# Kernel tuning notes

Measured on AMD Instinct MI355X. Metric: run time of the kernel, lower is better.

Reference implementation:

```python
import jax, jax.numpy as jnp
import numpy as np

NS = 100000  # senders
NR = 100000  # receivers
E = 600000   # edges
D = 128      # sender_dim = receiver_dim = edge_dim
EPS = 1e-5


def _layer_norm(x, g, b):
    mu = jnp.mean(x, axis=-1, keepdims=True)
    var = jnp.mean(jnp.square(x - mu), axis=-1, keepdims=True)
    return (x - mu) * jax.lax.rsqrt(var + EPS) * g + b


def _gcast_mlp(x, W, b, gamma, beta):
    # Faithful to GCastMLP.forward: z = silu(linear(x)); z = LN(silu(z))
    z = jax.nn.silu(x @ W.T + b)
    return _layer_norm(jax.nn.silu(z), gamma, beta)


def setup_inputs() -> dict:
    key = jax.random.key(0)
    ks = jax.random.split(key, 12)
    s = 1.0 / np.sqrt(3 * D)
    inp = {
        "sender_x": jax.random.normal(ks[0], (NS, D), jnp.float32),
        "receiver_x": jax.random.normal(ks[1], (NR, D), jnp.float32),
        "edge_index": jax.random.randint(ks[2], (2, E), 0, NR, jnp.int32),
        "edge_attr": jax.random.normal(ks[3], (E, D), jnp.float32),
        # edge MLP: in = sender+receiver+edge = 3D, out = edge_dim
        "We": jax.random.uniform(ks[4], (D, 3 * D), jnp.float32, -s, s),
        "be": jnp.zeros((D,), jnp.float32),
        "ge": jnp.ones((D,), jnp.float32),
        "bbe": jnp.zeros((D,), jnp.float32),
        # node MLP: in = receiver+edge = 2D, out = receiver_dim
        "Wn": jax.random.uniform(ks[5], (D, 2 * D), jnp.float32, -1.0 / np.sqrt(2 * D), 1.0 / np.sqrt(2 * D)),
        "bn": jnp.zeros((D,), jnp.float32),
        "gn": jnp.ones((D,), jnp.float32),
        "bbn": jnp.zeros((D,), jnp.float32),
        # sender MLP: square D -> D
        "Ws": jax.random.uniform(ks[6], (D, D), jnp.float32, -1.0 / np.sqrt(D), 1.0 / np.sqrt(D)),
        "bs": jnp.zeros((D,), jnp.float32),
        "gs": jnp.ones((D,), jnp.float32),
        "bbs": jnp.zeros((D,), jnp.float32),
    }
    return inp


def reference(sender_x, receiver_x, edge_index, edge_attr,
              We, be, ge, bbe, Wn, bn, gn, bbn, Ws, bs, gs, bbs):
    src, dst = edge_index[0], edge_index[1]
    # Edge encoder: gather endpoints, concat, MLP -> new edge features [E, D]
    edge_in = jnp.concatenate([sender_x[src], receiver_x[dst], edge_attr], axis=-1)
    edge_attr_p = _gcast_mlp(edge_in, We, be, ge, bbe)
    # Node encoder: scatter-sum messages (= new edge features) to receivers
    edge_aggr = jax.ops.segment_sum(edge_attr_p, dst, num_segments=receiver_x.shape[0])
    mesh_x_p = _gcast_mlp(jnp.concatenate([receiver_x, edge_aggr], axis=-1), Wn, bn, gn, bbn)
    # Residual updates
    sender_out = sender_x + _gcast_mlp(sender_x, Ws, bs, gs, bbs)
    receiver_out = receiver_x + mesh_x_p
    edge_out = edge_attr + edge_attr_p
    return (sender_out, receiver_out, edge_out)
```

## Files before the change

kernel.cpp:

```cpp
#include <hip/hip_runtime.h>
#include <stdint.h>


typedef __bf16 bf16x8 __attribute__((ext_vector_type(8)));
typedef float  f32x4  __attribute__((ext_vector_type(4)));

union U16B { uint4 u; bf16x8 v; };
union BFPK { __bf16 h[2]; unsigned int u; };
union BF1  { __bf16 h; unsigned short s; };

__device__ __forceinline__ float silu_f(float x) {
  return x * __builtin_amdgcn_rcpf(1.0f + __expf(-x));
}
__device__ __forceinline__ float bfu2f(unsigned int lo16) {
  return __uint_as_float(lo16 << 16);
}
__device__ __forceinline__ bf16x8 cvt8(float4 a, float4 b) {
  bf16x8 r;
  r[0] = (__bf16)a.x; r[1] = (__bf16)a.y; r[2] = (__bf16)a.z; r[3] = (__bf16)a.w;
  r[4] = (__bf16)b.x; r[5] = (__bf16)b.y; r[6] = (__bf16)b.z; r[7] = (__bf16)b.w;
  return r;
}

__global__ void prep_kernel(const float* __restrict__ We,
                            const float* __restrict__ Wn,
                            const float* __restrict__ Ws,
                            unsigned short* __restrict__ wimg,
                            const float* __restrict__ sx,
                            unsigned short* __restrict__ sb,
                            const float* __restrict__ rx,
                            unsigned short* __restrict__ rb,
                            int n8s, int n8r,
                            const int* __restrict__ dst,
                            int* __restrict__ counts, int E) {
  int i = blockIdx.x * 256 + threadIdx.x;
  if (i < 6 * 16384) {
    int panel = i >> 14;
    int r = (i >> 7) & 127;
    int csw = i & 127;
    int c_or = ((csw * 2) ^ ((r & 15) << 4)) >> 1;
    float f;
    if (panel < 3)      f = We[r * 384 + panel * 128 + c_or];
    else if (panel < 5) f = Wn[r * 256 + (panel - 3) * 128 + c_or];
    else                f = Ws[r * 128 + c_or];
    BF1 c; c.h = (__bf16)f;
    wimg[i] = c.s;
    return;
  }
  int j = i - 6 * 16384;
  if (j < n8s + n8r) {
    const float* in; unsigned short* out; int idx;
    if (j < n8s) { in = sx; out = sb; idx = j; }
    else         { in = rx; out = rb; idx = j - n8s; }
    float4 a = reinterpret_cast<const float4*>(in)[2 * idx];
    float4 b = reinterpret_cast<const float4*>(in)[2 * idx + 1];
    U16B r8; r8.v = cvt8(a, b);
    reinterpret_cast<uint4*>(out)[idx] = r8.u;
    return;
  }
  int e = j - n8s - n8r;
  if (e < E) atomicAdd(&counts[dst[e]], 1);
}

__global__ void scan1_kernel(const int* __restrict__ counts, int* __restrict__ pre,
                             int* __restrict__ blockSums, int n) {
  __shared__ int sh[256];
  const int t = threadIdx.x;
  const int base = blockIdx.x * 1024 + t * 4;
  int c0 = (base + 0 < n) ? counts[base + 0] : 0;
  int c1 = (base + 1 < n) ? counts[base + 1] : 0;
  int c2 = (base + 2 < n) ? counts[base + 2] : 0;
  int c3 = (base + 3 < n) ? counts[base + 3] : 0;
  int tot = c0 + c1 + c2 + c3;
  sh[t] = tot;
  __syncthreads();
  #pragma unroll
  for (int off = 1; off < 256; off <<= 1) {
    int v = (t >= off) ? sh[t - off] : 0;
    __syncthreads();
    sh[t] += v;
    __syncthreads();
  }
  int excl = sh[t] - tot;
  if (base + 0 < n) pre[base + 0] = excl;
  if (base + 1 < n) pre[base + 1] = excl + c0;
  if (base + 2 < n) pre[base + 2] = excl + c0 + c1;
  if (base + 3 < n) pre[base + 3] = excl + c0 + c1 + c2;
  if (t == 255) blockSums[blockIdx.x] = sh[255];
}

__global__ void scan2_kernel(int* __restrict__ blockSums, int nb) {
  __shared__ int sh[512];
  const int t = threadIdx.x;
  int v = (t < nb) ? blockSums[t] : 0;
  sh[t] = v;
  __syncthreads();
  #pragma unroll
  for (int off = 1; off < 512; off <<= 1) {
    int u = (t >= off) ? sh[t - off] : 0;
    __syncthreads();
    sh[t] += u;
    __syncthreads();
  }
  if (t < nb) blockSums[t] = sh[t] - v;
}

__global__ void scan3_kernel(const int* __restrict__ pre, const int* __restrict__ blockSums,
                             int* __restrict__ offs, int* __restrict__ cursor, int n) {
  int i = blockIdx.x * 256 + threadIdx.x;
  if (i >= n) return;
  int o = pre[i] + blockSums[i >> 10];
  offs[i] = o;
  cursor[i] = o;
}

__global__ void scatter_kernel(const int* __restrict__ dst, int* __restrict__ cursor,
                               int* __restrict__ rank, int E) {
  int i = blockIdx.x * 256 + threadIdx.x;
  if (i < E) {
    int p = atomicAdd(&cursor[dst[i]], 1);
    rank[i] = p;
  }
}

__global__ __launch_bounds__(256) void agg_kernel(
    const unsigned short* __restrict__ P,
    const int* __restrict__ offs, const int* __restrict__ counts,
    unsigned short* __restrict__ aggr, int NR) {
  const int l = threadIdx.x & 31;
  const int g0 = (blockIdx.x * 256 + threadIdx.x) >> 5;
  if (g0 >= NR) return;
  int beg = offs[g0];
  int cnt = counts[g0];
  float s0 = 0.f, s1 = 0.f, s2 = 0.f, s3 = 0.f;
  const unsigned short* p = P + (size_t)beg * 128 + l * 4;
  for (int k = 0; k < cnt; ++k) {
    uint2 w = *reinterpret_cast<const uint2*>(p);
    p += 128;
    s0 += bfu2f(w.x & 0xffffu);
    s1 += bfu2f(w.x >> 16);
    s2 += bfu2f(w.y & 0xffffu);
    s3 += bfu2f(w.y >> 16);
  }
  BFPK a, b;
  a.h[0] = (__bf16)s0; a.h[1] = (__bf16)s1;
  b.h[0] = (__bf16)s2; b.h[1] = (__bf16)s3;
  uint2 o; o.x = a.u; o.y = b.u;
  *reinterpret_cast<uint2*>(aggr + (size_t)g0 * 128 + l * 4) = o;
}

template <int KDIM, int AGGR>
__global__ __launch_bounds__(512, 6) void mlp_v10_kernel(
    const unsigned short* __restrict__ s0, const int* __restrict__ i0,
    const unsigned short* __restrict__ s1, const int* __restrict__ i1,
    const float* __restrict__ s2,
    const unsigned short* __restrict__ Wb,
    const float* __restrict__ bias, const float* __restrict__ gamma,
    const float* __restrict__ beta,
    const float* __restrict__ resid,
    float* __restrict__ outp,
    void* aggr, const int* __restrict__ aggr_idx,
    const int* __restrict__ prank,
    int M) {
  constexpr int NSEG = KDIM / 128;
  __shared__ __align__(16) unsigned short smem[16384];

  const int tid = threadIdx.x;
  const int wid = tid >> 6;
  const int lane = tid & 63;
  const int l15 = lane & 15;
  const int q = lane >> 4;
  const int l31 = lane & 31;
  const int rhalf = lane >> 5;
  const int wrow = blockIdx.x * 128 + wid * 16;
  const int xm = l15 << 3;

  int rr = wrow + l15;
  if (rr >= M) rr = M - 1;
  const unsigned short* p0 = s0 + (size_t)(i0 ? i0[rr] : rr) * 128;
  const unsigned short* p1 = nullptr;
  const float* p2 = nullptr;
  if constexpr (KDIM >= 256) p1 = s1 + (size_t)(i1 ? i1[rr] : rr) * 128;
  if constexpr (KDIM >= 384) p2 = s2 + (size_t)rr * 128;

  auto stageB = [&](int seg) {
    const unsigned short* g = Wb + seg * 16384 + wid * 2048 + lane * 8;
    unsigned short* l = &smem[wid * 2048];
    #pragma unroll
    for (int u = 0; u < 4; ++u) {
      __builtin_amdgcn_global_load_lds(
          (const __attribute__((address_space(1))) unsigned int*)(g + u * 512),
          (__attribute__((address_space(3))) unsigned int*)(l + u * 512),
          16, 0, 0);
    }
  };

  U16B Ac[4], An[4];
  auto loadA = [&](int seg, U16B (&dst)[4]) {
    #pragma unroll
    for (int k4 = 0; k4 < 4; ++k4) {
      const int kof = k4 * 32 + q * 8;
      if (seg == 0) {
        dst[k4].u = *reinterpret_cast<const uint4*>(p0 + kof);
      } else if (seg == 1) {
        dst[k4].u = *reinterpret_cast<const uint4*>(p1 + kof);
      } else {
        const float4* p = reinterpret_cast<const float4*>(p2 + kof);
        dst[k4].v = cvt8(p[0], p[1]);
      }
    }
  };

  f32x4 acc[8] = {};

  stageB(0);
  loadA(0, Ac);
  __syncthreads();

  #pragma unroll
  for (int seg = 0; seg < NSEG; ++seg) {
    if (seg + 1 < NSEG) loadA(seg + 1, An);
    #pragma unroll
    for (int k4 = 0; k4 < 4; ++k4) {
      #pragma unroll
      for (int n = 0; n < 8; ++n) {
        U16B b;
        b.u = *reinterpret_cast<const uint4*>(
            &smem[(n * 16 + l15) * 128 + ((k4 * 32 + q * 8) ^ xm)]);
        acc[n] = __builtin_amdgcn_mfma_f32_16x16x32_bf16(Ac[k4].v, b.v, acc[n], 0, 0, 0);
      }
    }
    __syncthreads();
    if (seg + 1 < NSEG) {
      stageB(seg + 1);
      __syncthreads();
      #pragma unroll
      for (int k4 = 0; k4 < 4; ++k4) Ac[k4] = An[k4];
    }
  }

  float bia[8];
  #pragma unroll
  for (int n = 0; n < 8; ++n) bia[n] = bias[n * 16 + l15];

  float sum[4] = {0.f, 0.f, 0.f, 0.f};
  float ssq[4] = {0.f, 0.f, 0.f, 0.f};
  #pragma unroll
  for (int n = 0; n < 8; ++n) {
    #pragma unroll
    for (int j = 0; j < 4; ++j) {
      float t = silu_f(silu_f(acc[n][j] + bia[n]));
      acc[n][j] = t;
      sum[j] += t;
      ssq[j] += t * t;
    }
  }
  #pragma unroll
  for (int off = 1; off < 16; off <<= 1) {
    #pragma unroll
    for (int j = 0; j < 4; ++j) {
      sum[j] += __shfl_xor(sum[j], off);
      ssq[j] += __shfl_xor(ssq[j], off);
    }
  }
  float mu[4], rs[4];
  #pragma unroll
  for (int j = 0; j < 4; ++j) {
    mu[j] = sum[j] * (1.0f / 128.0f);
    float var = ssq[j] * (1.0f / 128.0f) - mu[j] * mu[j];
    rs[j] = rsqrtf(var + 1e-5f);
  }
  float gam[8], bet[8];
  #pragma unroll
  for (int n = 0; n < 8; ++n) {
    gam[n] = gamma[n * 16 + l15];
    bet[n] = beta[n * 16 + l15];
  }

  unsigned short* yw = &smem[wid * 2048];

  #pragma unroll
  for (int h = 0; h < 2; ++h) {
    if (h == 1) {
      asm volatile("s_waitcnt lgkmcnt(0)" ::: "memory");
    }
    if ((q >> 1) == h) {
      #pragma unroll
      for (int n = 0; n < 8; ++n) {
        #pragma unroll
        for (int j = 0; j < 4; ++j) {
          float y = (acc[n][j] - mu[j]) * rs[j] * gam[n] + bet[n];
          BF1 c; c.h = (__bf16)y;
          yw[((q & 1) * 4 + j) * 132 + n * 16 + l15] = c.s;
        }
      }
    }
    asm volatile("s_waitcnt lgkmcnt(0)" ::: "memory");

    #pragma unroll
    for (int s = 0; s < 4; ++s) {
      int row8 = 2 * s + rhalf;
      int grow = wrow + 8 * h + row8;
      uint2 w = *reinterpret_cast<const uint2*>(&yw[row8 * 132 + l31 * 4]);
      if (grow < M) {
        const f32x4 r4 = *reinterpret_cast<const f32x4*>(resid + (size_t)grow * 128 + l31 * 4);
        f32x4 o4;
        o4.x = r4.x + bfu2f(w.x & 0xffffu);
        o4.y = r4.y + bfu2f(w.x >> 16);
        o4.z = r4.z + bfu2f(w.y & 0xffffu);
        o4.w = r4.w + bfu2f(w.y >> 16);
        __builtin_nontemporal_store(o4, reinterpret_cast<f32x4*>(outp + (size_t)grow * 128 + l31 * 4));
        if constexpr (AGGR == 3) {
          int prow = prank[grow];
          *reinterpret_cast<uint2*>((unsigned short*)aggr + (size_t)prow * 128 + l31 * 4) = w;
        } else if constexpr (AGGR == 2) {
          int idx = aggr_idx[grow];
          unsigned short* ar = (unsigned short*)aggr + (size_t)idx * 128 + l31 * 4;
          asm volatile("global_atomic_pk_add_bf16 %0, %1, off" :: "v"(ar), "v"(w.x) : "memory");
          asm volatile("global_atomic_pk_add_bf16 %0, %1, off" :: "v"(ar + 2), "v"(w.y) : "memory");
        }
      }
    }
  }
}

template <int KDIM>
__global__ __launch_bounds__(512, 4) void mlp_fb_kernel(
    const float* __restrict__ s0, const int* __restrict__ i0,
    const float* __restrict__ s1, const int* __restrict__ i1,
    const float* __restrict__ s2,
    const unsigned short* __restrict__ Wb,
    const float* __restrict__ bias, const float* __restrict__ gamma,
    const float* __restrict__ beta,
    const float* __restrict__ resid,
    float* __restrict__ outp,
    float* aggr, const int* __restrict__ aggr_idx,
    int M) {
  constexpr int NSEG = KDIM / 128;
  __shared__ __align__(16) unsigned short smem[2][16384];
  const int tid = threadIdx.x;
  const int wid = tid >> 6;
  const int lane = tid & 63;
  const int l15 = lane & 15;
  const int q = lane >> 4;
  const int l31 = lane & 31;
  const int rhalf = lane >> 5;
  const int wrow = blockIdx.x * 128 + wid * 16;
  const int xm = l15 << 3;

  int rr = wrow + l15;
  if (rr >= M) rr = M - 1;
  const float* p0 = s0 + (size_t)(i0 ? i0[rr] : rr) * 128;
  const float* p1 = (KDIM >= 256) ? (s1 + (size_t)(i1 ? i1[rr] : rr) * 128) : nullptr;
  const float* p2 = (KDIM >= 384) ? (s2 + (size_t)rr * 128) : nullptr;

  auto stageB = [&](int seg, int buf) {
    const unsigned short* g = Wb + seg * 16384 + wid * 2048 + lane * 8;
    unsigned short* l = &smem[buf][wid * 2048];
    #pragma unroll
    for (int u = 0; u < 4; ++u) {
      __builtin_amdgcn_global_load_lds(
          (const __attribute__((address_space(1))) unsigned int*)(g + u * 512),
          (__attribute__((address_space(3))) unsigned int*)(l + u * 512),
          16, 0, 0);
    }
  };

  stageB(0, 0);
  f32x4 acc[8] = {};
  __syncthreads();
  int cur = 0;
  #pragma unroll
  for (int seg = 0; seg < NSEG; ++seg) {
    if (seg + 1 < NSEG) stageB(seg + 1, cur ^ 1);
    const float* base = (seg == 0) ? p0 : ((seg == 1) ? p1 : p2);
    #pragma unroll
    for (int k4 = 0; k4 < 4; ++k4) {
      const float4* pp = reinterpret_cast<const float4*>(base + k4 * 32 + q * 8);
      U16B a; a.v = cvt8(pp[0], pp[1]);
      #pragma unroll
      for (int n = 0; n < 8; ++n) {
        U16B b;
        b.u = *reinterpret_cast<const uint4*>(
            &smem[cur][(n * 16 + l15) * 128 + ((k4 * 32 + q * 8) ^ xm)]);
        acc[n] = __builtin_amdgcn_mfma_f32_16x16x32_bf16(a.v, b.v, acc[n], 0, 0, 0);
      }
    }
    __syncthreads();
    if (seg + 1 < NSEG) cur ^= 1;
  }

  unsigned short* yw = &smem[0][0] + wid * (16 * 132);
  float bia[8];
  #pragma unroll
  for (int n = 0; n < 8; ++n) bia[n] = bias[n * 16 + l15];
  float sum[4] = {0.f, 0.f, 0.f, 0.f}, ssq[4] = {0.f, 0.f, 0.f, 0.f};
  #pragma unroll
  for (int n = 0; n < 8; ++n)
    #pragma unroll
    for (int j = 0; j < 4; ++j) {
      float t = silu_f(silu_f(acc[n][j] + bia[n]));
      acc[n][j] = t; sum[j] += t; ssq[j] += t * t;
    }
  #pragma unroll
  for (int off = 1; off < 16; off <<= 1)
    #pragma unroll
    for (int j = 0; j < 4; ++j) {
      sum[j] += __shfl_xor(sum[j], off);
      ssq[j] += __shfl_xor(ssq[j], off);
    }
  float mu[4], rs[4];
  #pragma unroll
  for (int j = 0; j < 4; ++j) {
    mu[j] = sum[j] * (1.0f / 128.0f);
    float var = ssq[j] * (1.0f / 128.0f) - mu[j] * mu[j];
    rs[j] = rsqrtf(var + 1e-5f);
  }
  float gam[8], bet[8];
  #pragma unroll
  for (int n = 0; n < 8; ++n) { gam[n] = gamma[n * 16 + l15]; bet[n] = beta[n * 16 + l15]; }
  #pragma unroll
  for (int n = 0; n < 8; ++n)
    #pragma unroll
    for (int j = 0; j < 4; ++j) {
      float y = (acc[n][j] - mu[j]) * rs[j] * gam[n] + bet[n];
      BF1 c; c.h = (__bf16)y;
      yw[(q * 4 + j) * 132 + n * 16 + l15] = c.s;
    }
  asm volatile("s_waitcnt lgkmcnt(0)" ::: "memory");
  #pragma unroll
  for (int s = 0; s < 8; ++s) {
    int row16 = 2 * s + rhalf;
    int grow = wrow + row16;
    uint2 w = *reinterpret_cast<const uint2*>(&yw[row16 * 132 + l31 * 4]);
    if (grow < M) {
      const f32x4 r4 = *reinterpret_cast<const f32x4*>(resid + (size_t)grow * 128 + l31 * 4);
      f32x4 o4;
      o4.x = r4.x + bfu2f(w.x & 0xffffu);
      o4.y = r4.y + bfu2f(w.x >> 16);
      o4.z = r4.z + bfu2f(w.y & 0xffffu);
      o4.w = r4.w + bfu2f(w.y >> 16);
      __builtin_nontemporal_store(o4, reinterpret_cast<f32x4*>(outp + (size_t)grow * 128 + l31 * 4));
      if (aggr) {
        int idx = aggr_idx[grow];
        float* ar = aggr + (size_t)idx * 128 + l31 * 4;
        atomicAdd(ar + 0, bfu2f(w.x & 0xffffu));
        atomicAdd(ar + 1, bfu2f(w.x >> 16));
        atomicAdd(ar + 2, bfu2f(w.y & 0xffffu));
        atomicAdd(ar + 3, bfu2f(w.y >> 16));
      }
    }
  }
}

extern "C" void kernel_launch(void* const* d_in, const int* in_sizes, int n_in,
                              void* d_out, int out_size, void* d_ws, size_t ws_size,
                              hipStream_t stream) {
  const float* sender_x   = (const float*)d_in[0];
  const float* receiver_x = (const float*)d_in[1];
  const int*   edge_index = (const int*)d_in[2];
  const float* edge_attr  = (const float*)d_in[3];
  const float* We  = (const float*)d_in[4];
  const float* be  = (const float*)d_in[5];
  const float* ge  = (const float*)d_in[6];
  const float* bbe = (const float*)d_in[7];
  const float* Wn  = (const float*)d_in[8];
  const float* bn  = (const float*)d_in[9];
  const float* gn  = (const float*)d_in[10];
  const float* bbn = (const float*)d_in[11];
  const float* Ws  = (const float*)d_in[12];
  const float* bs  = (const float*)d_in[13];
  const float* gs  = (const float*)d_in[14];
  const float* bbs = (const float*)d_in[15];

  const int D  = 128;
  const int NS = in_sizes[0] / D;
  const int NR = in_sizes[1] / D;
  const int E  = in_sizes[2] / 2;

  const int* src = edge_index;
  const int* dst = edge_index + E;

  float* out          = (float*)d_out;
  float* sender_out   = out;
  float* receiver_out = out + (size_t)NS * D;
  float* edge_out     = out + (size_t)(NS + NR) * D;

  const size_t welems = 6 * 16384;
  unsigned short* We_b = (unsigned short*)d_ws;
  unsigned short* Wn_b = We_b + 3 * 16384;
  unsigned short* Ws_b = We_b + 5 * 16384;
  unsigned short* sender_b   = We_b + welems;
  unsigned short* receiver_b = sender_b + (size_t)NS * D;
  unsigned short* aggr_b     = receiver_b + (size_t)NR * D;
  unsigned short* P_b        = aggr_b + (size_t)NR * D;
  int* counts    = (int*)(P_b + (size_t)E * D);
  int* pre       = counts + NR;
  int* offs      = pre + NR;
  int* cursor    = offs + NR;
  int* blockSums = cursor + NR;
  int* rank      = blockSums + 512;

  const int nScanBlocks = (NR + 1023) / 1024;
  const size_t needCSR = 2 * (welems + (size_t)(NS + 2 * NR) * D + (size_t)E * D)
                       + 4 * (4 * (size_t)NR + 512 + (size_t)E);
  const size_t needA = (welems + (size_t)(NS + 2 * NR) * D) * 2;

  int tier;
  if (ws_size >= needCSR && nScanBlocks <= 512) tier = 0;
  else if (ws_size >= needA) tier = 1;
  else tier = 2;

  const int gridE = (E + 127) / 128;
  const int gridR = (NR + 127) / 128;
  const int gridS = (NS + 127) / 128;
  const int n8s = NS * D / 8, n8r = NR * D / 8;

  if (tier == 0) {
    (void)hipMemsetAsync(counts, 0, (size_t)NR * 4, stream);
    const int prepItems = (int)welems + n8s + n8r + E;
    prep_kernel<<<(prepItems + 255) / 256, 256, 0, stream>>>(
        We, Wn, Ws, We_b, sender_x, sender_b, receiver_x, receiver_b,
        n8s, n8r, dst, counts, E);

    scan1_kernel<<<nScanBlocks, 256, 0, stream>>>(counts, pre, blockSums, NR);
    scan2_kernel<<<1, 512, 0, stream>>>(blockSums, nScanBlocks);
    scan3_kernel<<<(NR + 255) / 256, 256, 0, stream>>>(pre, blockSums, offs, cursor, NR);
    scatter_kernel<<<(E + 255) / 256, 256, 0, stream>>>(dst, cursor, rank, E);

    mlp_v10_kernel<384, 3><<<gridE, 512, 0, stream>>>(
        sender_b, src, receiver_b, dst, edge_attr,
        We_b, be, ge, bbe, edge_attr, edge_out, P_b, nullptr, rank, E);

    agg_kernel<<<(NR + 7) / 8, 256, 0, stream>>>(P_b, offs, counts, aggr_b, NR);

    mlp_v10_kernel<256, 0><<<gridR, 512, 0, stream>>>(
        receiver_b, nullptr, aggr_b, nullptr, nullptr,
        Wn_b, bn, gn, bbn, receiver_x, receiver_out, nullptr, nullptr, nullptr, NR);

    mlp_v10_kernel<128, 0><<<gridS, 512, 0, stream>>>(
        sender_b, nullptr, nullptr, nullptr, nullptr,
        Ws_b, bs, gs, bbs, sender_x, sender_out, nullptr, nullptr, nullptr, NS);
  } else if (tier == 1) {
    const int prepItems = (int)welems + n8s + n8r;
    prep_kernel<<<(prepItems + 255) / 256, 256, 0, stream>>>(
        We, Wn, Ws, We_b, sender_x, sender_b, receiver_x, receiver_b,
        n8s, n8r, nullptr, nullptr, 0);
    (void)hipMemsetAsync(aggr_b, 0, (size_t)NR * D * 2, stream);

    mlp_v10_kernel<384, 2><<<gridE, 512, 0, stream>>>(
        sender_b, src, receiver_b, dst, edge_attr,
        We_b, be, ge, bbe, edge_attr, edge_out, aggr_b, dst, nullptr, E);

    mlp_v10_kernel<256, 0><<<gridR, 512, 0, stream>>>(
        receiver_b, nullptr, aggr_b, nullptr, nullptr,
        Wn_b, bn, gn, bbn, receiver_x, receiver_out, nullptr, nullptr, nullptr, NR);

    mlp_v10_kernel<128, 0><<<gridS, 512, 0, stream>>>(
        sender_b, nullptr, nullptr, nullptr, nullptr,
        Ws_b, bs, gs, bbs, sender_x, sender_out, nullptr, nullptr, nullptr, NS);
  } else {
    prep_kernel<<<(int)((welems + 255) / 256), 256, 0, stream>>>(
        We, Wn, Ws, We_b, nullptr, nullptr, nullptr, nullptr, 0, 0,
        nullptr, nullptr, 0);
    (void)hipMemsetAsync(receiver_out, 0, (size_t)NR * D * sizeof(float), stream);

    mlp_fb_kernel<384><<<gridE, 512, 0, stream>>>(
        sender_x, src, receiver_x, dst, edge_attr,
        We_b, be, ge, bbe, edge_attr, edge_out, receiver_out, dst, E);

    mlp_fb_kernel<256><<<gridR, 512, 0, stream>>>(
        receiver_x, nullptr, receiver_out, nullptr, nullptr,
        Wn_b, bn, gn, bbn, receiver_x, receiver_out, nullptr, nullptr, NR);

    mlp_fb_kernel<128><<<gridS, 512, 0, stream>>>(
        sender_x, nullptr, nullptr, nullptr, nullptr,
        Ws_b, bs, gs, bbs, sender_x, sender_out, nullptr, nullptr, NS);
  }
}
```

Measured before the change: 450.0 us.

## Precompute sender/receiver projections per node before edge MLP gather

Splits the edge linear layer by linearity: the sender and receiver blocks of We are applied once per node (100k rows each) in a new pregemm kernel, writing bf16 projections. The edge kernel then runs only a K=128 GEMM on edge_attr and adds gathered precomputed projections, instead of a K=384 GEMM on gathered raw features for 600k edges. This cuts edge MFMA work to a third. In exchange it adds an extra kernel, extra workspace, and a second bf16 rounding of the projected sender and receiver terms.

```diff
diff --git a/kernel.cpp b/kernel.cpp
--- a/kernel.cpp
+++ b/kernel.cpp
@@ -149,6 +149,189 @@
   *reinterpret_cast<uint2*>(aggr + (size_t)g0 * 128 + l * 4) = o;
 }
 
+__global__ __launch_bounds__(512, 4) void pregemm_kernel(
+    const unsigned short* __restrict__ Xs, const unsigned short* __restrict__ Xr,
+    const unsigned short* __restrict__ Wp0, const unsigned short* __restrict__ Wp1,
+    unsigned short* __restrict__ Sp, unsigned short* __restrict__ Rp,
+    int NSl, int NRl, int gridS) {
+  __shared__ __align__(16) unsigned short smem[16384];
+  const bool isR = ((int)blockIdx.x >= gridS);
+  const unsigned short* X  = isR ? Xr : Xs;
+  const unsigned short* Wp = isR ? Wp1 : Wp0;
+  unsigned short* OUT = isR ? Rp : Sp;
+  const int M = isR ? NRl : NSl;
+  const int b = isR ? ((int)blockIdx.x - gridS) : (int)blockIdx.x;
+
+  const int tid = threadIdx.x;
+  const int wid = tid >> 6;
+  const int lane = tid & 63;
+  const int l15 = lane & 15;
+  const int q = lane >> 4;
+  const int xm = l15 << 3;
+
+  int e = b * 128 + wid * 16 + l15;
+  const bool valid = (e < M);
+  if (!valid) e = M - 1;
+
+  {
+    const unsigned short* g = Wp + wid * 2048 + lane * 8;
+    unsigned short* l = &smem[wid * 2048];
+    #pragma unroll
+    for (int u = 0; u < 4; ++u) {
+      __builtin_amdgcn_global_load_lds(
+          (const __attribute__((address_space(1))) unsigned int*)(g + u * 512),
+          (__attribute__((address_space(3))) unsigned int*)(l + u * 512),
+          16, 0, 0);
+    }
+  }
+
+  U16B bfr[4];
+  const unsigned short* xp = X + (size_t)e * 128;
+  #pragma unroll
+  for (int k4 = 0; k4 < 4; ++k4)
+    bfr[k4].u = *reinterpret_cast<const uint4*>(xp + k4 * 32 + q * 8);
+
+  __syncthreads();
+
+  f32x4 acc[8] = {};
+  #pragma unroll
+  for (int k4 = 0; k4 < 4; ++k4) {
+    #pragma unroll
+    for (int n = 0; n < 8; ++n) {
+      U16B a;
+      a.u = *reinterpret_cast<const uint4*>(
+          &smem[(n * 16 + l15) * 128 + ((k4 * 32 + q * 8) ^ xm)]);
+      acc[n] = __builtin_amdgcn_mfma_f32_16x16x32_bf16(a.v, bfr[k4].v, acc[n], 0, 0, 0);
+    }
+  }
+
+  if (valid) {
+    #pragma unroll
+    for (int n = 0; n < 8; ++n) {
+      BFPK k0, k1;
+      k0.h[0] = (__bf16)acc[n][0]; k0.h[1] = (__bf16)acc[n][1];
+      k1.h[0] = (__bf16)acc[n][2]; k1.h[1] = (__bf16)acc[n][3];
+      uint2 w; w.x = k0.u; w.y = k1.u;
+      *reinterpret_cast<uint2*>(OUT + (size_t)e * 128 + n * 16 + q * 4) = w;
+    }
+  }
+}
+
+__global__ __launch_bounds__(512, 4) void edge_v11_kernel(
+    const float* __restrict__ edge_attr,
+    const int* __restrict__ src, const int* __restrict__ dst,
+    const unsigned short* __restrict__ Sp, const unsigned short* __restrict__ Rp,
+    const unsigned short* __restrict__ Wp,
+    const float* __restrict__ bias, const float* __restrict__ gamma,
+    const float* __restrict__ beta,
+    float* __restrict__ edge_out,
+    unsigned short* __restrict__ P, const int* __restrict__ prank,
+    int E) {
+  __shared__ __align__(16) unsigned short smem[16384];
+  const int tid = threadIdx.x;
+  const int wid = tid >> 6;
+  const int lane = tid & 63;
+  const int l15 = lane & 15;
+  const int q = lane >> 4;
+  const int xm = l15 << 3;
+
+  int e = blockIdx.x * 128 + wid * 16 + l15;
+  const bool valid = (e < E);
+  if (!valid) e = E - 1;
+
+  {
+    const unsigned short* g = Wp + wid * 2048 + lane * 8;
+    unsigned short* l = &smem[wid * 2048];
+    #pragma unroll
+    for (int u = 0; u < 4; ++u) {
+      __builtin_amdgcn_global_load_lds(
+          (const __attribute__((address_space(1))) unsigned int*)(g + u * 512),
+          (__attribute__((address_space(3))) unsigned int*)(l + u * 512),
+          16, 0, 0);
+    }
+  }
+
+  const float* ep = edge_attr + (size_t)e * 128;
+  U16B bfr[4];
+  #pragma unroll
+  for (int k4 = 0; k4 < 4; ++k4) {
+    const float4* p = reinterpret_cast<const float4*>(ep + k4 * 32 + q * 8);
+    bfr[k4].v = cvt8(p[0], p[1]);
+  }
+
+  const int se = src[e];
+  const int de = dst[e];
+  const int rk = prank[e];
+  uint2 Sg[8], Rg[8];
+  const unsigned short* sp = Sp + (size_t)se * 128 + q * 4;
+  const unsigned short* rp = Rp + (size_t)de * 128 + q * 4;
+  #pragma unroll
+  for (int n = 0; n < 8; ++n) {
+    Sg[n] = *reinterpret_cast<const uint2*>(sp + n * 16);
+    Rg[n] = *reinterpret_cast<const uint2*>(rp + n * 16);
+  }
+
+  __syncthreads();
+
+  f32x4 acc[8] = {};
+  #pragma unroll
+  for (int k4 = 0; k4 < 4; ++k4) {
+    #pragma unroll
+    for (int n = 0; n < 8; ++n) {
+      U16B a;
+      a.u = *reinterpret_cast<const uint4*>(
+          &smem[(n * 16 + l15) * 128 + ((k4 * 32 + q * 8) ^ xm)]);
+      acc[n] = __builtin_amdgcn_mfma_f32_16x16x32_bf16(a.v, bfr[k4].v, acc[n], 0, 0, 0);
+    }
+  }
+
+  float sum = 0.f, ssq = 0.f;
+  #pragma unroll
+  for (int n = 0; n < 8; ++n) {
+    const f32x4 b4 = *reinterpret_cast<const f32x4*>(bias + n * 16 + q * 4);
+    float sg0 = bfu2f(Sg[n].x & 0xffffu), sg1 = bfu2f(Sg[n].x >> 16);
+    float sg2 = bfu2f(Sg[n].y & 0xffffu), sg3 = bfu2f(Sg[n].y >> 16);
+    float rg0 = bfu2f(Rg[n].x & 0xffffu), rg1 = bfu2f(Rg[n].x >> 16);
+    float rg2 = bfu2f(Rg[n].y & 0xffffu), rg3 = bfu2f(Rg[n].y >> 16);
+    float z0 = acc[n][0] + b4[0] + sg0 + rg0;
+    float z1 = acc[n][1] + b4[1] + sg1 + rg1;
+    float z2 = acc[n][2] + b4[2] + sg2 + rg2;
+    float z3 = acc[n][3] + b4[3] + sg3 + rg3;
+    float t0 = silu_f(silu_f(z0));
+    float t1 = silu_f(silu_f(z1));
+    float t2 = silu_f(silu_f(z2));
+    float t3 = silu_f(silu_f(z3));
+    acc[n][0] = t0; acc[n][1] = t1; acc[n][2] = t2; acc[n][3] = t3;
+    sum += (t0 + t1) + (t2 + t3);
+    ssq += (t0 * t0 + t1 * t1) + (t2 * t2 + t3 * t3);
+  }
+  sum += __shfl_xor(sum, 16); ssq += __shfl_xor(ssq, 16);
+  sum += __shfl_xor(sum, 32); ssq += __shfl_xor(ssq, 32);
+  const float mu = sum * (1.0f / 128.0f);
+  const float rs = rsqrtf(ssq * (1.0f / 128.0f) - mu * mu + 1e-5f);
+
+  #pragma unroll
+  for (int n = 0; n < 8; ++n) {
+    const f32x4 g4  = *reinterpret_cast<const f32x4*>(gamma + n * 16 + q * 4);
+    const f32x4 be4 = *reinterpret_cast<const f32x4*>(beta + n * 16 + q * 4);
+    const f32x4 r4  = *reinterpret_cast<const f32x4*>(ep + n * 16 + q * 4);
+    f32x4 y;
+    #pragma unroll
+    for (int j = 0; j < 4; ++j)
+      y[j] = (acc[n][j] - mu) * rs * g4[j] + be4[j];
+    if (valid) {
+      f32x4 o4 = r4 + y;
+      __builtin_nontemporal_store(
+          o4, reinterpret_cast<f32x4*>(edge_out + (size_t)e * 128 + n * 16 + q * 4));
+      BFPK k0, k1;
+      k0.h[0] = (__bf16)y[0]; k0.h[1] = (__bf16)y[1];
+      k1.h[0] = (__bf16)y[2]; k1.h[1] = (__bf16)y[3];
+      uint2 w; w.x = k0.u; w.y = k1.u;
+      *reinterpret_cast<uint2*>(P + (size_t)rk * 128 + n * 16 + q * 4) = w;
+    }
+  }
+}
+
 template <int KDIM, int AGGR>
 __global__ __launch_bounds__(512, 6) void mlp_v10_kernel(
     const unsigned short* __restrict__ s0, const int* __restrict__ i0,
@@ -500,23 +683,27 @@
   int* cursor    = offs + NR;
   int* blockSums = cursor + NR;
   int* rank      = blockSums + 512;
+  unsigned short* Sp = (unsigned short*)(rank + E);
+  unsigned short* Rp = Sp + (size_t)NS * D;
 
   const int nScanBlocks = (NR + 1023) / 1024;
   const size_t needCSR = 2 * (welems + (size_t)(NS + 2 * NR) * D + (size_t)E * D)
                        + 4 * (4 * (size_t)NR + 512 + (size_t)E);
+  const size_t needCSR2 = needCSR + 2 * ((size_t)(NS + NR) * D);
   const size_t needA = (welems + (size_t)(NS + 2 * NR) * D) * 2;
 
   int tier;
-  if (ws_size >= needCSR && nScanBlocks <= 512) tier = 0;
-  else if (ws_size >= needA) tier = 1;
-  else tier = 2;
+  if (ws_size >= needCSR2 && nScanBlocks <= 512) tier = 0;
+  else if (ws_size >= needCSR && nScanBlocks <= 512) tier = 1;
+  else if (ws_size >= needA) tier = 2;
+  else tier = 3;
 
   const int gridE = (E + 127) / 128;
   const int gridR = (NR + 127) / 128;
   const int gridS = (NS + 127) / 128;
   const int n8s = NS * D / 8, n8r = NR * D / 8;
 
-  if (tier == 0) {
+  if (tier <= 1) {
     (void)hipMemsetAsync(counts, 0, (size_t)NR * 4, stream);
     const int prepItems = (int)welems + n8s + n8r + E;
     prep_kernel<<<(prepItems + 255) / 256, 256, 0, stream>>>(
@@ -528,9 +715,18 @@
     scan3_kernel<<<(NR + 255) / 256, 256, 0, stream>>>(pre, blockSums, offs, cursor, NR);
     scatter_kernel<<<(E + 255) / 256, 256, 0, stream>>>(dst, cursor, rank, E);
 
-    mlp_v10_kernel<384, 3><<<gridE, 512, 0, stream>>>(
-        sender_b, src, receiver_b, dst, edge_attr,
-        We_b, be, ge, bbe, edge_attr, edge_out, P_b, nullptr, rank, E);
+    if (tier == 0) {
+      pregemm_kernel<<<gridS + gridR, 512, 0, stream>>>(
+          sender_b, receiver_b, We_b, We_b + 16384, Sp, Rp, NS, NR, gridS);
+
+      edge_v11_kernel<<<gridE, 512, 0, stream>>>(
+          edge_attr, src, dst, Sp, Rp, We_b + 2 * 16384,
+          be, ge, bbe, edge_out, P_b, rank, E);
+    } else {
+      mlp_v10_kernel<384, 3><<<gridE, 512, 0, stream>>>(
+          sender_b, src, receiver_b, dst, edge_attr,
+          We_b, be, ge, bbe, edge_attr, edge_out, P_b, nullptr, rank, E);
+    }
 
     agg_kernel<<<(NR + 7) / 8, 256, 0, stream>>>(P_b, offs, counts, aggr_b, NR);
 
@@ -541,7 +737,7 @@
     mlp_v10_kernel<128, 0><<<gridS, 512, 0, stream>>>(
         sender_b, nullptr, nullptr, nullptr, nullptr,
         Ws_b, bs, gs, bbs, sender_x, sender_out, nullptr, nullptr, nullptr, NS);
-  } else if (tier == 1) {
+  } else if (tier == 2) {
     const int prepItems = (int)welems + n8s + n8r;
     prep_kernel<<<(prepItems + 255) / 256, 256, 0, stream>>>(
         We, Wn, Ws, We_b, sender_x, sender_b, receiver_x, receiver_b,
```

New measurement: 537.3 us. 19.4% more time.

## Fuse CSR aggregation into node MLP and merge edge and sender MLP launches

Applied to the files above, without the earlier changes.

Removes the separate agg_kernel and instead gathers each receiver's CSR-sorted edge messages directly into the A-operand registers of a new node MLP kernel, which skips writing and re-reading the bf16 aggregate buffer. The receiver-half GEMM is issued first so the second weight segment can load while the aggregation loop runs. The edge MLP and sender MLP are also merged into one launch that picks its path by block index, cutting launches and filling the tail of the edge grid. In exchange, the node kernel does one per-row gather loop per lane group with uneven degree across rows, uses more registers (launch bounds 512,4), and may have lower memory-level parallelism than the old dedicated aggregation kernel.

```diff
diff --git a/kernel.cpp b/kernel.cpp
--- a/kernel.cpp
+++ b/kernel.cpp
@@ -123,34 +123,9 @@
   }
 }
 
-__global__ __launch_bounds__(256) void agg_kernel(
-    const unsigned short* __restrict__ P,
-    const int* __restrict__ offs, const int* __restrict__ counts,
-    unsigned short* __restrict__ aggr, int NR) {
-  const int l = threadIdx.x & 31;
-  const int g0 = (blockIdx.x * 256 + threadIdx.x) >> 5;
-  if (g0 >= NR) return;
-  int beg = offs[g0];
-  int cnt = counts[g0];
-  float s0 = 0.f, s1 = 0.f, s2 = 0.f, s3 = 0.f;
-  const unsigned short* p = P + (size_t)beg * 128 + l * 4;
-  for (int k = 0; k < cnt; ++k) {
-    uint2 w = *reinterpret_cast<const uint2*>(p);
-    p += 128;
-    s0 += bfu2f(w.x & 0xffffu);
-    s1 += bfu2f(w.x >> 16);
-    s2 += bfu2f(w.y & 0xffffu);
-    s3 += bfu2f(w.y >> 16);
-  }
-  BFPK a, b;
-  a.h[0] = (__bf16)s0; a.h[1] = (__bf16)s1;
-  b.h[0] = (__bf16)s2; b.h[1] = (__bf16)s3;
-  uint2 o; o.x = a.u; o.y = b.u;
-  *reinterpret_cast<uint2*>(aggr + (size_t)g0 * 128 + l * 4) = o;
-}
-
 template <int KDIM, int AGGR>
-__global__ __launch_bounds__(512, 6) void mlp_v10_kernel(
+__device__ __forceinline__ void mlp_core(
+    unsigned short* smem,
     const unsigned short* __restrict__ s0, const int* __restrict__ i0,
     const unsigned short* __restrict__ s1, const int* __restrict__ i1,
     const float* __restrict__ s2,
@@ -161,9 +136,8 @@
     float* __restrict__ outp,
     void* aggr, const int* __restrict__ aggr_idx,
     const int* __restrict__ prank,
-    int M) {
+    int M, int bid) {
   constexpr int NSEG = KDIM / 128;
-  __shared__ __align__(16) unsigned short smem[16384];
 
   const int tid = threadIdx.x;
   const int wid = tid >> 6;
@@ -172,7 +146,7 @@
   const int q = lane >> 4;
   const int l31 = lane & 31;
   const int rhalf = lane >> 5;
-  const int wrow = blockIdx.x * 128 + wid * 16;
+  const int wrow = bid * 128 + wid * 16;
   const int xm = l15 << 3;
 
   int rr = wrow + l15;
@@ -319,6 +293,229 @@
           asm volatile("global_atomic_pk_add_bf16 %0, %1, off" :: "v"(ar), "v"(w.x) : "memory");
           asm volatile("global_atomic_pk_add_bf16 %0, %1, off" :: "v"(ar + 2), "v"(w.y) : "memory");
         }
+      }
+    }
+  }
+}
+
+template <int KDIM, int AGGR>
+__global__ __launch_bounds__(512, 6) void mlp_v10_kernel(
+    const unsigned short* __restrict__ s0, const int* __restrict__ i0,
+    const unsigned short* __restrict__ s1, const int* __restrict__ i1,
+    const float* __restrict__ s2,
+    const unsigned short* __restrict__ Wb,
+    const float* __restrict__ bias, const float* __restrict__ gamma,
+    const float* __restrict__ beta,
+    const float* __restrict__ resid,
+    float* __restrict__ outp,
+    void* aggr, const int* __restrict__ aggr_idx,
+    const int* __restrict__ prank,
+    int M) {
+  __shared__ __align__(16) unsigned short smem[16384];
+  mlp_core<KDIM, AGGR>(smem, s0, i0, s1, i1, s2, Wb, bias, gamma, beta,
+                       resid, outp, aggr, aggr_idx, prank, M, blockIdx.x);
+}
+
+__global__ __launch_bounds__(512, 6) void fused_es_kernel(
+    const unsigned short* __restrict__ sender_b, const int* __restrict__ src,
+    const unsigned short* __restrict__ receiver_b, const int* __restrict__ dst,
+    const float* __restrict__ edge_attr,
+    const unsigned short* __restrict__ We_b,
+    const float* __restrict__ be, const float* __restrict__ ge,
+    const float* __restrict__ bbe,
+    float* __restrict__ edge_out,
+    unsigned short* __restrict__ P, const int* __restrict__ rank,
+    const unsigned short* __restrict__ Ws_b,
+    const float* __restrict__ bs, const float* __restrict__ gs,
+    const float* __restrict__ bbs,
+    const float* __restrict__ sender_x, float* __restrict__ sender_out,
+    int E, int NS, int gridE) {
+  __shared__ __align__(16) unsigned short smem[16384];
+  const int b = blockIdx.x;
+  if (b < gridE) {
+    mlp_core<384, 3>(smem, sender_b, src, receiver_b, dst, edge_attr,
+                     We_b, be, ge, bbe, edge_attr, edge_out,
+                     P, nullptr, rank, E, b);
+  } else {
+    mlp_core<128, 0>(smem, sender_b, nullptr, nullptr, nullptr, nullptr,
+                     Ws_b, bs, gs, bbs, sender_x, sender_out,
+                     nullptr, nullptr, nullptr, NS, b - gridE);
+  }
+}
+
+__global__ __launch_bounds__(512, 4) void node_csr_kernel(
+    const unsigned short* __restrict__ s0,
+    const unsigned short* __restrict__ P,
+    const int* __restrict__ offs, const int* __restrict__ counts,
+    const unsigned short* __restrict__ Wb,
+    const float* __restrict__ bias, const float* __restrict__ gamma,
+    const float* __restrict__ beta,
+    const float* __restrict__ resid, float* __restrict__ outp,
+    int M) {
+  __shared__ __align__(16) unsigned short smem[16384];
+
+  const int tid = threadIdx.x;
+  const int wid = tid >> 6;
+  const int lane = tid & 63;
+  const int l15 = lane & 15;
+  const int q = lane >> 4;
+  const int l31 = lane & 31;
+  const int rhalf = lane >> 5;
+  const int wrow = blockIdx.x * 128 + wid * 16;
+  const int xm = l15 << 3;
+
+  int rr = wrow + l15;
+  if (rr >= M) rr = M - 1;
+  const unsigned short* p0 = s0 + (size_t)rr * 128;
+
+  auto stageB = [&](int seg) {
+    const unsigned short* g = Wb + seg * 16384 + wid * 2048 + lane * 8;
+    unsigned short* l = &smem[wid * 2048];
+    #pragma unroll
+    for (int u = 0; u < 4; ++u) {
+      __builtin_amdgcn_global_load_lds(
+          (const __attribute__((address_space(1))) unsigned int*)(g + u * 512),
+          (__attribute__((address_space(3))) unsigned int*)(l + u * 512),
+          16, 0, 0);
+    }
+  };
+
+  U16B Ac[4];
+  #pragma unroll
+  for (int k4 = 0; k4 < 4; ++k4)
+    Ac[k4].u = *reinterpret_cast<const uint4*>(p0 + k4 * 32 + q * 8);
+
+  stageB(0);
+  __syncthreads();
+
+  f32x4 acc[8] = {};
+  #pragma unroll
+  for (int k4 = 0; k4 < 4; ++k4) {
+    #pragma unroll
+    for (int n = 0; n < 8; ++n) {
+      U16B b;
+      b.u = *reinterpret_cast<const uint4*>(
+          &smem[(n * 16 + l15) * 128 + ((k4 * 32 + q * 8) ^ xm)]);
+      acc[n] = __builtin_amdgcn_mfma_f32_16x16x32_bf16(Ac[k4].v, b.v, acc[n], 0, 0, 0);
+    }
+  }
+  __syncthreads();
+  stageB(1);
+
+  {
+    int beg = offs[rr];
+    int cnt = counts[rr];
+    float a32[32];
+    #pragma unroll
+    for (int t = 0; t < 32; ++t) a32[t] = 0.f;
+    const unsigned short* prow = P + (size_t)beg * 128;
+    for (int k = 0; k < cnt; ++k) {
+      #pragma unroll
+      for (int k4 = 0; k4 < 4; ++k4) {
+        uint4 w = *reinterpret_cast<const uint4*>(prow + k4 * 32 + q * 8);
+        a32[k4 * 8 + 0] += bfu2f(w.x & 0xffffu);
+        a32[k4 * 8 + 1] += bfu2f(w.x >> 16);
+        a32[k4 * 8 + 2] += bfu2f(w.y & 0xffffu);
+        a32[k4 * 8 + 3] += bfu2f(w.y >> 16);
+        a32[k4 * 8 + 4] += bfu2f(w.z & 0xffffu);
+        a32[k4 * 8 + 5] += bfu2f(w.z >> 16);
+        a32[k4 * 8 + 6] += bfu2f(w.w & 0xffffu);
+        a32[k4 * 8 + 7] += bfu2f(w.w >> 16);
+      }
+      prow += 128;
+    }
+    #pragma unroll
+    for (int k4 = 0; k4 < 4; ++k4) {
+      #pragma unroll
+      for (int j = 0; j < 8; ++j)
+        Ac[k4].v[j] = (__bf16)a32[k4 * 8 + j];
+    }
+  }
+  __syncthreads();
+
+  #pragma unroll
+  for (int k4 = 0; k4 < 4; ++k4) {
+    #pragma unroll
+    for (int n = 0; n < 8; ++n) {
+      U16B b;
+      b.u = *reinterpret_cast<const uint4*>(
+          &smem[(n * 16 + l15) * 128 + ((k4 * 32 + q * 8) ^ xm)]);
+      acc[n] = __builtin_amdgcn_mfma_f32_16x16x32_bf16(Ac[k4].v, b.v, acc[n], 0, 0, 0);
+    }
+  }
+  __syncthreads();
+
+  float bia[8];
+  #pragma unroll
+  for (int n = 0; n < 8; ++n) bia[n] = bias[n * 16 + l15];
+
+  float sum[4] = {0.f, 0.f, 0.f, 0.f};
+  float ssq[4] = {0.f, 0.f, 0.f, 0.f};
+  #pragma unroll
+  for (int n = 0; n < 8; ++n) {
+    #pragma unroll
+    for (int j = 0; j < 4; ++j) {
+      float t = silu_f(silu_f(acc[n][j] + bia[n]));
+      acc[n][j] = t;
+      sum[j] += t;
+      ssq[j] += t * t;
+    }
+  }
+  #pragma unroll
+  for (int off = 1; off < 16; off <<= 1) {
+    #pragma unroll
+    for (int j = 0; j < 4; ++j) {
+      sum[j] += __shfl_xor(sum[j], off);
+      ssq[j] += __shfl_xor(ssq[j], off);
+    }
+  }
+  float mu[4], rs[4];
+  #pragma unroll
+  for (int j = 0; j < 4; ++j) {
+    mu[j] = sum[j] * (1.0f / 128.0f);
+    float var = ssq[j] * (1.0f / 128.0f) - mu[j] * mu[j];
+    rs[j] = rsqrtf(var + 1e-5f);
+  }
+  float gam[8], bet[8];
+  #pragma unroll
+  for (int n = 0; n < 8; ++n) {
+    gam[n] = gamma[n * 16 + l15];
+    bet[n] = beta[n * 16 + l15];
+  }
+
+  unsigned short* yw = &smem[wid * 2048];
+
+  #pragma unroll
+  for (int h = 0; h < 2; ++h) {
+    if (h == 1) {
+      asm volatile("s_waitcnt lgkmcnt(0)" ::: "memory");
+    }
+    if ((q >> 1) == h) {
+      #pragma unroll
+      for (int n = 0; n < 8; ++n) {
+        #pragma unroll
+        for (int j = 0; j < 4; ++j) {
+          float y = (acc[n][j] - mu[j]) * rs[j] * gam[n] + bet[n];
+          BF1 c; c.h = (__bf16)y;
+          yw[((q & 1) * 4 + j) * 132 + n * 16 + l15] = c.s;
+        }
+      }
+    }
+    asm volatile("s_waitcnt lgkmcnt(0)" ::: "memory");
+
+    #pragma unroll
+    for (int s = 0; s < 4; ++s) {
+      int row8 = 2 * s + rhalf;
+      int grow = wrow + 8 * h + row8;
+      uint2 w = *reinterpret_cast<const uint2*>(&yw[row8 * 132 + l31 * 4]);
+      if (grow < M) {
+        const f32x4 r4 = *reinterpret_cast<const f32x4*>(resid + (size_t)grow * 128 + l31 * 4);
+        f32x4 o4;
+        o4.x = r4.x + bfu2f(w.x & 0xffffu);
+        o4.y = r4.y + bfu2f(w.x >> 16);
+        o4.z = r4.z + bfu2f(w.y & 0xffffu);
+        o4.w = r4.w + bfu2f(w.y >> 16);
+        __builtin_nontemporal_store(o4, reinterpret_cast<f32x4*>(outp + (size_t)grow * 128 + l31 * 4));
       }
     }
   }
@@ -528,19 +725,15 @@
     scan3_kernel<<<(NR + 255) / 256, 256, 0, stream>>>(pre, blockSums, offs, cursor, NR);
     scatter_kernel<<<(E + 255) / 256, 256, 0, stream>>>(dst, cursor, rank, E);
 
-    mlp_v10_kernel<384, 3><<<gridE, 512, 0, stream>>>(
+    fused_es_kernel<<<gridE + gridS, 512, 0, stream>>>(
         sender_b, src, receiver_b, dst, edge_attr,
-        We_b, be, ge, bbe, edge_attr, edge_out, P_b, nullptr, rank, E);
-
-    agg_kernel<<<(NR + 7) / 8, 256, 0, stream>>>(P_b, offs, counts, aggr_b, NR);
-
-    mlp_v10_kernel<256, 0><<<gridR, 512, 0, stream>>>(
-        receiver_b, nullptr, aggr_b, nullptr, nullptr,
-        Wn_b, bn, gn, bbn, receiver_x, receiver_out, nullptr, nullptr, nullptr, NR);
-
-    mlp_v10_kernel<128, 0><<<gridS, 512, 0, stream>>>(
-        sender_b, nullptr, nullptr, nullptr, nullptr,
-        Ws_b, bs, gs, bbs, sender_x, sender_out, nullptr, nullptr, nullptr, NS);
+        We_b, be, ge, bbe, edge_out, P_b, rank,
+        Ws_b, bs, gs, bbs, sender_x, sender_out,
+        E, NS, gridE);
+
+    node_csr_kernel<<<gridR, 512, 0, stream>>>(
+        receiver_b, P_b, offs, counts,
+        Wn_b, bn, gn, bbn, receiver_x, receiver_out, NR);
   } else if (tier == 1) {
     const int prepItems = (int)welems + n8s + n8r;
     prep_kernel<<<(prepItems + 255) / 256, 256, 0, stream>>>(
```

Measured after the change: 451.4 us, median of 3. No clear change (+0.3%).
